# Performance work log

Measured on AMD Instinct MI355X. Metric: run time of the kernel, lower is better.

Reference implementation:

```python
import jax, jax.numpy as jnp
import numpy as np

K, STRIDE, PAD, DIL = 3, 1, 1, 1


def setup_inputs() -> dict:
    key = jax.random.key(0)
    k0, k1, k2, k3, k4 = jax.random.split(key, 5)
    B, Cin, Cout, H, W = 16, 64, 64, 64, 64
    x = jax.random.normal(k0, (B, Cin, H, W), dtype=jnp.float32)
    # NOTE: the torch module zero-inits conv_offset; we use small random
    # weights so the deformable sampling path is actually exercised.
    w_off = jax.random.normal(k1, (2 * K * K, Cin, K, K), dtype=jnp.float32) * 0.01
    b_off = jax.random.normal(k2, (2 * K * K,), dtype=jnp.float32) * 0.01
    fan_in = Cin * K * K
    w_dcn = jax.random.normal(k3, (Cout, Cin, K, K), dtype=jnp.float32) / np.sqrt(fan_in)
    b_dcn = jax.random.normal(k4, (Cout,), dtype=jnp.float32) * 0.01
    return {"x": x, "w_off": w_off, "b_off": b_off, "w_dcn": w_dcn, "b_dcn": b_dcn}


def _conv2d(x, w, b, stride, pad):
    out = jax.lax.conv_general_dilated(
        x, w, window_strides=(stride, stride), padding=[(pad, pad), (pad, pad)],
        dimension_numbers=("NCHW", "OIHW", "NCHW"))
    return out + b[None, :, None, None]


def _deform_conv(x, offset, w, b, stride, pad, dil):
    # torchvision-style DeformConv2d, groups=1, no modulation mask.
    B, Cin, H, W = x.shape
    Cout = w.shape[0]
    Ho = (H + 2 * pad - dil * (K - 1) - 1) // stride + 1
    Wo = (W + 2 * pad - dil * (K - 1) - 1) // stride + 1
    KK = K * K
    # base sampling grid: p0 + dilation*kernel_tap + learned offset
    oy = (jnp.arange(Ho) * stride - pad).astype(x.dtype)
    ox = (jnp.arange(Wo) * stride - pad).astype(x.dtype)
    ky, kx = jnp.meshgrid(jnp.arange(K), jnp.arange(K), indexing="ij")
    ky = (ky * dil).reshape(-1).astype(x.dtype)  # [KK], row (y) of tap
    kx = (kx * dil).reshape(-1).astype(x.dtype)
    # offset channel layout: [y_0, x_0, y_1, x_1, ...] -> [B, KK, 2, Ho, Wo]
    off = offset.reshape(B, KK, 2, Ho, Wo)
    py = off[:, :, 0] + ky[None, :, None, None] + oy[None, None, :, None]  # [B,KK,Ho,Wo]
    px = off[:, :, 1] + kx[None, :, None, None] + ox[None, None, None, :]
    y0 = jnp.floor(py)
    x0 = jnp.floor(px)
    wy1 = py - y0
    wx1 = px - x0
    wy0 = 1.0 - wy1
    wx0 = 1.0 - wx1
    x_flat = x.reshape(B, Cin, H * W)

    def gather(yi, xi):
        valid = (yi >= 0) & (yi < H) & (xi >= 0) & (xi < W)  # zero padding outside
        yc = jnp.clip(yi, 0, H - 1).astype(jnp.int32)
        xc = jnp.clip(xi, 0, W - 1).astype(jnp.int32)
        idx = (yc * W + xc).reshape(B, 1, -1)
        v = jnp.take_along_axis(x_flat, idx, axis=2).reshape(B, Cin, KK, Ho, Wo)
        return v * valid.astype(x.dtype).reshape(B, 1, KK, Ho, Wo)

    cols = (gather(y0, x0) * (wy0 * wx0)[:, None]
            + gather(y0, x0 + 1) * (wy0 * wx1)[:, None]
            + gather(y0 + 1, x0) * (wy1 * wx0)[:, None]
            + gather(y0 + 1, x0 + 1) * (wy1 * wx1)[:, None])  # [B,Cin,KK,Ho,Wo]
    out = jnp.einsum("bckhw,ock->bohw", cols, w.reshape(Cout, Cin, KK))
    return out + b[None, :, None, None]


def reference(x, w_off, b_off, w_dcn, b_dcn):
    offset = _conv2d(x, w_off, b_off, STRIDE, PAD)
    return _deform_conv(x, offset, w_dcn, b_dcn, STRIDE, PAD, DIL)
```

## Files before the change

kernel.cpp:

```cpp
#include <hip/hip_runtime.h>
#include <hip/hip_fp16.h>


#define KOFF 18
#define CTS  136
#define GSTR 33

#define W2T_HALFS    (18 * 64 * 32)
#define WOFF2T_HALFS (18 * 32 * 32)
#define W2T_BYTES    (W2T_HALFS * 2)
#define WOFF2T_OFF   W2T_BYTES
#define X_OFF        (W2T_BYTES + WOFF2T_HALFS * 2)
#define XH_BYTES     (16 * 64 * 64 * 64 * 2)
#define WS_NEED      (X_OFF + XH_BYTES)

typedef _Float16 half8 __attribute__((ext_vector_type(8)));
typedef float floatx4 __attribute__((ext_vector_type(4)));

union H8 { half8 v; __half2 h2[4]; uint4 u; };

__global__ void prep(const float* __restrict__ x,
                     const float* __restrict__ w_dcn,
                     const float* __restrict__ w_off,
                     _Float16* __restrict__ w2t,
                     _Float16* __restrict__ woff2t,
                     _Float16* __restrict__ xh) {
    const int bi = blockIdx.x;
    const int t  = threadIdx.x;
    if (bi < 1024) {
        const int b = bi >> 6, y = bi & 63;
        __shared__ __align__(16) _Float16 tile[64 * 72];
        const int xx = t & 63;
        const int c4 = t >> 6;
        const float* xp = x + (((size_t)b * 64) * 64 + y) * 64;
#pragma unroll
        for (int p = 0; p < 16; ++p) {
            int cin = p * 4 + c4;
            tile[xx * 72 + cin] = (_Float16)xp[(size_t)cin * 4096 + xx];
        }
        __syncthreads();
        const int oct = t & 7;
        const int xl  = t >> 3;
        _Float16* op = xh + ((((size_t)b * 64 + y) * 64) << 6);
#pragma unroll
        for (int p = 0; p < 2; ++p) {
            int xr = p * 32 + xl;
            half8 v = *(const half8*)&tile[xr * 72 + oct * 8];
            *(half8*)&op[(size_t)xr * 64 + oct * 8] = v;
        }
    } else {
        int e = (bi - 1024) * 256 + t;
        if (e < W2T_HALFS) {
            int kl = e & 31, co = (e >> 5) & 63, i = e >> 11;
            int tap = i >> 1, cin = (i & 1) * 32 + kl;
            w2t[e] = (_Float16)w_dcn[co * 576 + cin * 9 + tap];
        } else {
            int e2 = e - W2T_HALFS;
            int kl = e2 & 31, co = (e2 >> 5) & 31, i = e2 >> 10;
            int tap = i >> 1, cin = (i & 1) * 32 + kl;
            woff2t[e2] = (co < KOFF) ? (_Float16)w_off[co * 576 + cin * 9 + tap]
                                     : (_Float16)0.f;
        }
    }
}

__launch_bounds__(256, 4)
__global__ void dcn_main(const _Float16* __restrict__ xh,
                         const _Float16* __restrict__ w2t,
                         const _Float16* __restrict__ woff2t,
                         const float* __restrict__ b_off,
                         const float* __restrict__ b_dcn,
                         float* __restrict__ out) {
    const int bid = blockIdx.x;
    const int s   = bid >> 3;
    const int b   = ((bid & 7) << 1) | (s >> 7);
    const int ho  = (s >> 1) & 63;
    const int hlf = s & 1;
    const int t    = threadIdx.x;
    const int lane = t & 63;
    const int wid  = __builtin_amdgcn_readfirstlane(t >> 6);
    const int r    = lane & 15;
    const int q    = lane >> 4;
    const int gpx  = t >> 3;
    const int oct  = t & 7;
    const int pxg  = hlf * 32;

    __shared__ __align__(16) _Float16 colsT[2][32 * CTS];
    __shared__ __align__(16) float    offlds[KOFF * 32];
    __shared__ __align__(16) uint4    grecL[9 * GSTR];

    const _Float16* xb = xh + ((size_t)b << 18);
    const char* xpb = (const char*)xb;

    {
        floatx4 am = {0.f, 0.f, 0.f, 0.f};
        const int m = wid & 1, n = wid >> 1;

        auto loadS = [&](int tap) -> half8 {
            const int dy = tap / 3, dxk = tap - dy * 3;
            const int y  = ho + dy - 1;
            const int xc = pxg + gpx + dxk - 1;
            half8 v = {};
            if (((unsigned)y < 64u) && ((unsigned)xc < 64u))
                v = *(const half8*)&xb[(((size_t)y * 64 + xc) << 6) + oct * 8];
            return v;
        };
        auto loadWA = [&](int i) -> half8 {
            return *(const half8*)&woff2t[i * 1024 + (m * 16 + r) * 32 + q * 8];
        };

        {
            half8 s0 = loadS(0), s1 = loadS(1);
            *(half8*)&colsT[0][gpx * CTS + oct * 8]      = s0;
            *(half8*)&colsT[0][gpx * CTS + 64 + oct * 8] = s1;
        }
        __syncthreads();
#pragma unroll
        for (int p = 0; p < 5; ++p) {
            half8 sn0, sn1;
            if (p < 4) {
                sn0 = loadS(2 * p + 2);
                if (p < 3) sn1 = loadS(2 * p + 3);
            }
            const int nkg = (p < 4) ? 4 : 2;
#pragma unroll
            for (int kg = 0; kg < 4; ++kg) {
                if (kg < nkg) {
                    half8 a  = loadWA(4 * p + kg);
                    half8 bf = *(const half8*)&colsT[p & 1][(n * 16 + r) * CTS
                                                            + kg * 32 + q * 8];
                    am = __builtin_amdgcn_mfma_f32_16x16x32_f16(a, bf, am, 0, 0, 0);
                }
            }
            if (p < 4) {
                *(half8*)&colsT[(p + 1) & 1][gpx * CTS + oct * 8] = sn0;
                if (p < 3)
                    *(half8*)&colsT[(p + 1) & 1][gpx * CTS + 64 + oct * 8] = sn1;
                __syncthreads();
            }
        }
#pragma unroll
        for (int reg = 0; reg < 4; ++reg) {
            int co = m * 16 + q * 4 + reg;
            if (co < KOFF)
                offlds[co * 32 + n * 16 + r] = am[reg] + b_off[co];
        }
    }
    __syncthreads();

    for (int e = t; e < 9 * 32; e += 256) {
        int tap = e >> 5, px = e & 31;
        float offy = offlds[(2 * tap) * 32 + px];
        float offx = offlds[(2 * tap + 1) * 32 + px];
        float py  = offy + (float)(tap / 3) + (float)(ho - 1);
        float pxf = offx + (float)(tap % 3) + (float)(pxg + px - 1);
        float fy = floorf(py), fx = floorf(pxf);
        int y0 = (int)fy, x0 = (int)fx;
        float wy1 = py - fy, wx1 = pxf - fx;
        float wy0 = 1.f - wy1, wx0 = 1.f - wx1;
        bool y0ok = ((unsigned)y0 < 64u);
        bool x0ok = ((unsigned)x0 < 64u);
        bool y1ok = ((unsigned)(y0 + 1) < 64u);
        bool x1ok = ((unsigned)(x0 + 1) < 64u);
        float w00 = (y0ok && x0ok) ? wy0 * wx0 : 0.f;
        float w01 = (y0ok && x1ok) ? wy0 * wx1 : 0.f;
        float w10 = (y1ok && x0ok) ? wy1 * wx0 : 0.f;
        float w11 = (y1ok && x1ok) ? wy1 * wx1 : 0.f;
        int yc0 = min(max(y0, 0), 63);
        int xc0 = min(max(x0, 0), 63);
        int yc1 = min(max(y0 + 1, 0), 63);
        int xc1 = min(max(x0 + 1, 0), 63);
        union { __half2 h; unsigned u; } c0, c1;
        c0.h = __floats2half2_rn(w00, w01);
        c1.h = __floats2half2_rn(w10, w11);
        uint4 rec;
        rec.x = (unsigned)(yc0 * 64 + xc0)
              | ((unsigned)(xc1 - xc0) << 12)
              | ((unsigned)(yc1 - yc0) << 13);
        rec.y = c0.u;
        rec.z = c1.u;
        rec.w = 0u;
        grecL[tap * GSTR + px] = rec;
    }
    __syncthreads();

    floatx4 acc0 = {0.f, 0.f, 0.f, 0.f};
    floatx4 acc1 = {0.f, 0.f, 0.f, 0.f};

    struct GP { H8 v[8]; unsigned wy0, wz0, wy1, wz1; };

    auto loadPairB = [&](int p) -> GP {
        GP g;
#pragma unroll
        for (int l = 0; l < 2; ++l) {
            int tap = 2 * p + l;
            if (tap < 9) {
                uint4 rec = grecL[tap * GSTR + gpx];
                unsigned a00 = (rec.x & 0xfffu) * 128u + (unsigned)oct * 16u;
                unsigned dx128  = ((rec.x >> 12) & 1u) * 128u;
                unsigned dy8192 = ((rec.x >> 13) & 1u) * 8192u;
                g.v[4 * l + 0].v = *(const half8*)(xpb + a00);
                g.v[4 * l + 1].v = *(const half8*)(xpb + a00 + dx128);
                g.v[4 * l + 2].v = *(const half8*)(xpb + a00 + dy8192);
                g.v[4 * l + 3].v = *(const half8*)(xpb + a00 + dy8192 + dx128);
                if (l == 0) { g.wy0 = rec.y; g.wz0 = rec.z; }
                else        { g.wy1 = rec.y; g.wz1 = rec.z; }
            }
        }
        return g;
    };
    auto storePairB = [&](int p, int buf, GP& g) {
#pragma unroll
        for (int l = 0; l < 2; ++l) {
            int tap = 2 * p + l;
            if (tap < 9) {
                union { unsigned u; __half2 h; } cy, cz;
                cy.u = l ? g.wy1 : g.wy0;
                cz.u = l ? g.wz1 : g.wz0;
                __half2 W00 = __half2half2(__low2half(cy.h));
                __half2 W01 = __half2half2(__high2half(cy.h));
                __half2 W10 = __half2half2(__low2half(cz.h));
                __half2 W11 = __half2half2(__high2half(cz.h));
                H8 res;
#pragma unroll
                for (int c = 0; c < 4; ++c) {
                    __half2 aa = __hmul2(g.v[4 * l + 0].h2[c], W00);
                    aa = __hfma2(g.v[4 * l + 1].h2[c], W01, aa);
                    aa = __hfma2(g.v[4 * l + 2].h2[c], W10, aa);
                    aa = __hfma2(g.v[4 * l + 3].h2[c], W11, aa);
                    res.h2[c] = aa;
                }
                *(half8*)&colsT[buf][gpx * CTS + l * 64 + oct * 8] = res.v;
            }
        }
    };
    auto loadW = [&](int i) -> half8 {
        return *(const half8*)&w2t[(size_t)i * 2048 + (wid * 16 + r) * 32 + q * 8];
    };

    {
        GP g0 = loadPairB(0);
        storePairB(0, 0, g0);
    }
    half8 wf[4];
#pragma unroll
    for (int kg = 0; kg < 4; ++kg) wf[kg] = loadW(kg);
    __syncthreads();

#pragma unroll
    for (int p = 0; p < 5; ++p) {
        GP gn;
        half8 wfn[4];
        if (p < 4) {
            gn = loadPairB(p + 1);
#pragma unroll
            for (int kg = 0; kg < 4; ++kg)
                if (4 * (p + 1) + kg < 18) wfn[kg] = loadW(4 * (p + 1) + kg);
        }
        const int nkg = (p < 4) ? 4 : 2;
#pragma unroll
        for (int kg = 0; kg < 4; ++kg) {
            if (kg < nkg) {
                half8 b0 = *(const half8*)&colsT[p & 1][r * CTS + kg * 32 + q * 8];
                half8 b1 = *(const half8*)&colsT[p & 1][(16 + r) * CTS + kg * 32 + q * 8];
                acc0 = __builtin_amdgcn_mfma_f32_16x16x32_f16(wf[kg], b0, acc0, 0, 0, 0);
                acc1 = __builtin_amdgcn_mfma_f32_16x16x32_f16(wf[kg], b1, acc1, 0, 0, 0);
            }
        }
        if (p < 4) {
            storePairB(p + 1, (p + 1) & 1, gn);
#pragma unroll
            for (int kg = 0; kg < 4; ++kg) wf[kg] = wfn[kg];
            __syncthreads();
        }
    }

#pragma unroll
    for (int reg = 0; reg < 4; ++reg) {
        int co = wid * 16 + q * 4 + reg;
        float bias = b_dcn[co];
        size_t o = (((size_t)b * 64 + co) * 64 + ho) * 64 + pxg;
        out[o + r]      = acc0[reg] + bias;
        out[o + 16 + r] = acc1[reg] + bias;
    }
}

#define FCPAD 40
__launch_bounds__(256, 4)
__global__ void dcn_fb(const float* __restrict__ x,
                       const float* __restrict__ w_dcn,
                       const float* __restrict__ w_off,
                       const float* __restrict__ b_off,
                       const float* __restrict__ b_dcn,
                       float* __restrict__ out) {
    const int bid = blockIdx.x;
    const int s   = bid >> 3;
    const int b   = ((bid & 7) << 1) | (s >> 7);
    const int ho  = (s >> 1) & 63;
    const int hlf = s & 1;
    const int t    = threadIdx.x;
    const int lane = t & 63;
    const int wid  = __builtin_amdgcn_readfirstlane(t >> 6);
    const int r    = lane & 15;
    const int q    = lane >> 4;
    const int px   = t & 31;
    const int kq   = t >> 5;

    __shared__ __align__(16) _Float16 colsT[2][32 * FCPAD];
    __shared__ __align__(16) float    offlds[KOFF * 32];

    const float* xb = x + (size_t)b * 64 * 4096;
    const int pxg = hlf * 32;

    {
        floatx4 am = {0.f, 0.f, 0.f, 0.f};
        const int m = wid & 1, n = wid >> 1;
        auto stageA = [&](int i) {
            const int tap = i >> 1;
            const int dy = tap / 3, dxk = tap - dy * 3;
            const int y  = ho + dy - 1;
            const int xc = pxg + px + dxk - 1;
            const bool ok = ((unsigned)y < 64u) && ((unsigned)xc < 64u);
            const float* xp = xb + ((size_t)((i & 1) * 32 + kq * 4)) * 4096
                                 + y * 64 + xc;
            float va[4];
#pragma unroll
            for (int j = 0; j < 4; ++j) va[j] = ok ? xp[(size_t)j * 4096] : 0.f;
#pragma unroll
            for (int j = 0; j < 4; ++j)
                colsT[i & 1][px * FCPAD + kq * 4 + j] = (_Float16)va[j];
        };
        auto loadA = [&](int i) -> half8 {
            const int tap = i >> 1;
            const int cin0 = (i & 1) * 32 + q * 8;
            const int co = m * 16 + r;
            half8 v;
#pragma unroll
            for (int j = 0; j < 8; ++j)
                v[j] = (co < KOFF) ? (_Float16)w_off[co * 576 + (cin0 + j) * 9 + tap]
                                   : (_Float16)0.f;
            return v;
        };
        stageA(0);
        __syncthreads();
#pragma unroll
        for (int i = 0; i < 18; ++i) {
            if (i < 17) stageA(i + 1);
            half8 a = loadA(i);
            half8 bfr = *(const half8*)&colsT[i & 1][(n * 16 + r) * FCPAD + q * 8];
            am = __builtin_amdgcn_mfma_f32_16x16x32_f16(a, bfr, am, 0, 0, 0);
            __syncthreads();
        }
#pragma unroll
        for (int reg = 0; reg < 4; ++reg) {
            int co = m * 16 + q * 4 + reg;
            if (co < KOFF)
                offlds[co * 32 + (n * 16 + r)] = am[reg] + b_off[co];
        }
    }
    __syncthreads();

    unsigned rmeta[9], rw0[9], rw1[9];
#pragma unroll
    for (int tap = 0; tap < 9; ++tap) {
        float offy = offlds[(2 * tap) * 32 + px];
        float offx = offlds[(2 * tap + 1) * 32 + px];
        float py  = offy + (float)(tap / 3) + (float)(ho - 1);
        float pxf = offx + (float)(tap % 3) + (float)(pxg + px - 1);
        float fy = floorf(py), fx = floorf(pxf);
        int y0 = (int)fy, x0 = (int)fx;
        float wy1 = py - fy, wx1 = pxf - fx;
        float wy0 = 1.f - wy1, wx0 = 1.f - wx1;
        bool y0ok = ((unsigned)y0 < 64u);
        bool x0ok = ((unsigned)x0 < 64u);
        bool y1ok = ((unsigned)(y0 + 1) < 64u);
        bool x1ok = ((unsigned)(x0 + 1) < 64u);
        float w00 = (y0ok && x0ok) ? wy0 * wx0 : 0.f;
        float w01 = (y0ok && x1ok) ? wy0 * wx1 : 0.f;
        float w10 = (y1ok && x0ok) ? wy1 * wx0 : 0.f;
        float w11 = (y1ok && x1ok) ? wy1 * wx1 : 0.f;
        int yc0 = min(max(y0, 0), 63);
        int xc0 = min(max(x0, 0), 63);
        int yc1 = min(max(y0 + 1, 0), 63);
        int xc1 = min(max(x0 + 1, 0), 63);
        union { __half2 h; unsigned u; } c0, c1;
        c0.h = __floats2half2_rn(w00, w01);
        c1.h = __floats2half2_rn(w10, w11);
        rmeta[tap] = (unsigned)(yc0 * 64 + xc0)
                   | ((unsigned)(xc1 - xc0) << 12)
                   | ((unsigned)(yc1 - yc0) << 13);
        rw0[tap] = c0.u;
        rw1[tap] = c1.u;
    }

    floatx4 acc0 = {0.f, 0.f, 0.f, 0.f};
    floatx4 acc1 = {0.f, 0.f, 0.f, 0.f};

    auto gather = [&](int i) {
        const int tap = i >> 1;
        const unsigned m = rmeta[tap];
        const unsigned a00 = (m & 0xfffu) << 2;
        const unsigned a01 = a00 + ((m >> 10) & 4u);
        const unsigned a10 = a00 + ((m >> 5) & 256u);
        const unsigned a11 = a10 + ((m >> 10) & 4u);
        const char* base = (const char*)xb
                         + ((size_t)((i & 1) * 32 + kq * 4)) * 16384;
        float v00[4], v01[4], v10[4], v11[4];
#pragma unroll
        for (int j = 0; j < 4; ++j) {
            const char* xp = base + (size_t)j * 16384;
            v00[j] = *(const float*)(xp + a00);
            v01[j] = *(const float*)(xp + a01);
            v10[j] = *(const float*)(xp + a10);
            v11[j] = *(const float*)(xp + a11);
        }
        union { unsigned u; __half2 h; } c0, c1;
        c0.u = rw0[tap]; c1.u = rw1[tap];
        const float wA = __half2float(c0.h.x), wB = __half2float(c0.h.y);
        const float wC = __half2float(c1.h.x), wD = __half2float(c1.h.y);
#pragma unroll
        for (int j = 0; j < 4; ++j)
            colsT[i & 1][px * FCPAD + kq * 4 + j] =
                (_Float16)(v00[j] * wA + v01[j] * wB + v10[j] * wC + v11[j] * wD);
    };

    auto load_af = [&](int i) -> half8 {
        const int tap = i >> 1;
        const int cin0 = (i & 1) * 32 + q * 8;
        half8 v;
#pragma unroll
        for (int j = 0; j < 8; ++j)
            v[j] = (_Float16)w_dcn[(wid * 16 + r) * 576 + (cin0 + j) * 9 + tap];
        return v;
    };

    gather(0);
    __syncthreads();
#pragma unroll
    for (int i = 0; i < 18; ++i) {
        if (i < 17) gather(i + 1);
        half8 af = load_af(i);
        half8 b0 = *(const half8*)&colsT[i & 1][r * FCPAD + q * 8];
        half8 b1 = *(const half8*)&colsT[i & 1][(16 + r) * FCPAD + q * 8];
        acc0 = __builtin_amdgcn_mfma_f32_16x16x32_f16(af, b0, acc0, 0, 0, 0);
        acc1 = __builtin_amdgcn_mfma_f32_16x16x32_f16(af, b1, acc1, 0, 0, 0);
        if (i < 17) __syncthreads();
    }

#pragma unroll
    for (int reg = 0; reg < 4; ++reg) {
        int co = wid * 16 + q * 4 + reg;
        float bias = b_dcn[co];
        size_t o = (((size_t)b * 64 + co) * 64 + ho) * 64 + pxg;
        out[o + r]      = acc0[reg] + bias;
        out[o + 16 + r] = acc1[reg] + bias;
    }
}

extern "C" void kernel_launch(void* const* d_in, const int* in_sizes, int n_in,
                              void* d_out, int out_size, void* d_ws, size_t ws_size,
                              hipStream_t stream) {
    const float* x     = (const float*)d_in[0];
    const float* w_off = (const float*)d_in[1];
    const float* b_off = (const float*)d_in[2];
    const float* w_dcn = (const float*)d_in[3];
    const float* b_dcn = (const float*)d_in[4];
    float* out = (float*)d_out;

    char* ws = (char*)d_ws;
    _Float16* w2t    = (_Float16*)ws;
    _Float16* woff2t = (_Float16*)(ws + WOFF2T_OFF);
    _Float16* xh     = (_Float16*)(ws + X_OFF);

    if (ws_size >= (size_t)WS_NEED) {
        prep<<<1240, 256, 0, stream>>>(x, w_dcn, w_off, w2t, woff2t, xh);
        dcn_main<<<2048, 256, 0, stream>>>(xh, w2t, woff2t, b_off, b_dcn, out);
    } else {
        dcn_fb<<<2048, 256, 0, stream>>>(x, w_dcn, w_off, b_off, b_dcn, out);
    }
}
```

Measured before the change: 107.6 us.

## Prefetch gathers two stages ahead and use LDS-only barriers

New measurement: 108.5 us. About the same (+0.8%).

```diff
diff --git a/kernel.cpp b/kernel.cpp
--- a/kernel.cpp
+++ b/kernel.cpp
@@ -18,6 +18,11 @@
 typedef float floatx4 __attribute__((ext_vector_type(4)));
 
 union H8 { half8 v; __half2 h2[4]; uint4 u; };
+
+#define LBAR() do { \
+    asm volatile("s_waitcnt lgkmcnt(0)" ::: "memory"); \
+    __builtin_amdgcn_s_barrier(); \
+} while (0)
 
 __global__ void prep(const float* __restrict__ x,
                      const float* __restrict__ w_dcn,
@@ -109,19 +114,17 @@
             return *(const half8*)&woff2t[i * 1024 + (m * 16 + r) * 32 + q * 8];
         };
 
+        half8 t0, t1;
         {
             half8 s0 = loadS(0), s1 = loadS(1);
+            t0 = loadS(2);
+            t1 = loadS(3);
             *(half8*)&colsT[0][gpx * CTS + oct * 8]      = s0;
             *(half8*)&colsT[0][gpx * CTS + 64 + oct * 8] = s1;
         }
-        __syncthreads();
+        LBAR();
 #pragma unroll
         for (int p = 0; p < 5; ++p) {
-            half8 sn0, sn1;
-            if (p < 4) {
-                sn0 = loadS(2 * p + 2);
-                if (p < 3) sn1 = loadS(2 * p + 3);
-            }
             const int nkg = (p < 4) ? 4 : 2;
 #pragma unroll
             for (int kg = 0; kg < 4; ++kg) {
@@ -133,10 +136,14 @@
                 }
             }
             if (p < 4) {
-                *(half8*)&colsT[(p + 1) & 1][gpx * CTS + oct * 8] = sn0;
+                *(half8*)&colsT[(p + 1) & 1][gpx * CTS + oct * 8] = t0;
                 if (p < 3)
-                    *(half8*)&colsT[(p + 1) & 1][gpx * CTS + 64 + oct * 8] = sn1;
-                __syncthreads();
+                    *(half8*)&colsT[(p + 1) & 1][gpx * CTS + 64 + oct * 8] = t1;
+                if (p < 3) {
+                    t0 = loadS(2 * p + 4);
+                    if (p < 2) t1 = loadS(2 * p + 5);
+                }
+                LBAR();
             }
         }
 #pragma unroll
@@ -146,7 +153,7 @@
                 offlds[co * 32 + n * 16 + r] = am[reg] + b_off[co];
         }
     }
-    __syncthreads();
+    LBAR();
 
     for (int e = t; e < 9 * 32; e += 256) {
         int tap = e >> 5, px = e & 31;
@@ -182,7 +189,7 @@
         rec.w = 0u;
         grecL[tap * GSTR + px] = rec;
     }
-    __syncthreads();
+    LBAR();
 
     floatx4 acc0 = {0.f, 0.f, 0.f, 0.f};
     floatx4 acc1 = {0.f, 0.f, 0.f, 0.f};
@@ -242,17 +249,16 @@
         GP g0 = loadPairB(0);
         storePairB(0, 0, g0);
     }
+    GP gcur = loadPairB(1);
     half8 wf[4];
 #pragma unroll
     for (int kg = 0; kg < 4; ++kg) wf[kg] = loadW(kg);
-    __syncthreads();
+    LBAR();
 
 #pragma unroll
     for (int p = 0; p < 5; ++p) {
-        GP gn;
         half8 wfn[4];
         if (p < 4) {
-            gn = loadPairB(p + 1);
 #pragma unroll
             for (int kg = 0; kg < 4; ++kg)
                 if (4 * (p + 1) + kg < 18) wfn[kg] = loadW(4 * (p + 1) + kg);
@@ -268,10 +274,11 @@
             }
         }
         if (p < 4) {
-            storePairB(p + 1, (p + 1) & 1, gn);
+            storePairB(p + 1, (p + 1) & 1, gcur);
+            if (p < 3) gcur = loadPairB(p + 2);
 #pragma unroll
             for (int kg = 0; kg < 4; ++kg) wf[kg] = wfn[kg];
-            __syncthreads();
+            LBAR();
         }
     }
 
```

## Split offset conv into separate kernel and stage full im2col tile in LDS

Applied to the files above, without the earlier changes.

After: 110.8 us. +3.0%, slower.

```diff
diff --git a/kernel.cpp b/kernel.cpp
--- a/kernel.cpp
+++ b/kernel.cpp
@@ -4,7 +4,7 @@
 
 #define KOFF 18
 #define CTS  136
-#define GSTR 33
+#define CS9  584
 
 #define W2T_HALFS    (18 * 64 * 32)
 #define WOFF2T_HALFS (18 * 32 * 32)
@@ -12,7 +12,11 @@
 #define WOFF2T_OFF   W2T_BYTES
 #define X_OFF        (W2T_BYTES + WOFF2T_HALFS * 2)
 #define XH_BYTES     (16 * 64 * 64 * 64 * 2)
-#define WS_NEED      (X_OFF + XH_BYTES)
+#define GM_OFF       (X_OFF + XH_BYTES)
+#define GM_BYTES     (2048 * 288 * 4)
+#define GW_OFF       (GM_OFF + GM_BYTES)
+#define GW_BYTES     (2048 * 288 * 8)
+#define WS_NEED      (GW_OFF + GW_BYTES)
 
 typedef _Float16 half8 __attribute__((ext_vector_type(8)));
 typedef float floatx4 __attribute__((ext_vector_type(4)));
@@ -65,12 +69,11 @@
 }
 
 __launch_bounds__(256, 4)
-__global__ void dcn_main(const _Float16* __restrict__ xh,
-                         const _Float16* __restrict__ w2t,
-                         const _Float16* __restrict__ woff2t,
-                         const float* __restrict__ b_off,
-                         const float* __restrict__ b_dcn,
-                         float* __restrict__ out) {
+__global__ void offs_k(const _Float16* __restrict__ xh,
+                       const _Float16* __restrict__ woff2t,
+                       const float* __restrict__ b_off,
+                       unsigned int* __restrict__ gm,
+                       uint2* __restrict__ gw) {
     const int bid = blockIdx.x;
     const int s   = bid >> 3;
     const int b   = ((bid & 7) << 1) | (s >> 7);
@@ -87,10 +90,8 @@
 
     __shared__ __align__(16) _Float16 colsT[2][32 * CTS];
     __shared__ __align__(16) float    offlds[KOFF * 32];
-    __shared__ __align__(16) uint4    grecL[9 * GSTR];
 
     const _Float16* xb = xh + ((size_t)b << 18);
-    const char* xpb = (const char*)xb;
 
     {
         floatx4 am = {0.f, 0.f, 0.f, 0.f};
@@ -173,43 +174,78 @@
         union { __half2 h; unsigned u; } c0, c1;
         c0.h = __floats2half2_rn(w00, w01);
         c1.h = __floats2half2_rn(w10, w11);
-        uint4 rec;
-        rec.x = (unsigned)(yc0 * 64 + xc0)
-              | ((unsigned)(xc1 - xc0) << 12)
-              | ((unsigned)(yc1 - yc0) << 13);
-        rec.y = c0.u;
-        rec.z = c1.u;
-        rec.w = 0u;
-        grecL[tap * GSTR + px] = rec;
+        unsigned meta = (unsigned)(yc0 * 64 + xc0)
+                      | ((unsigned)(xc1 - xc0) << 12)
+                      | ((unsigned)(yc1 - yc0) << 13);
+        gm[(size_t)bid * 288 + e] = meta;
+        gw[(size_t)bid * 288 + e] = make_uint2(c0.u, c1.u);
+    }
+}
+
+__launch_bounds__(256, 4)
+__global__ void dcn_main(const _Float16* __restrict__ xh,
+                         const _Float16* __restrict__ w2t,
+                         const unsigned int* __restrict__ gm,
+                         const uint2* __restrict__ gw,
+                         const float* __restrict__ b_dcn,
+                         float* __restrict__ out) {
+    const int bid = blockIdx.x;
+    const int s   = bid >> 3;
+    const int b   = ((bid & 7) << 1) | (s >> 7);
+    const int ho  = (s >> 1) & 63;
+    const int hlf = s & 1;
+    const int t    = threadIdx.x;
+    const int lane = t & 63;
+    const int wid  = __builtin_amdgcn_readfirstlane(t >> 6);
+    const int r    = lane & 15;
+    const int q    = lane >> 4;
+    const int gpx  = t >> 3;
+    const int oct  = t & 7;
+    const int pxg  = hlf * 32;
+
+    __shared__ __align__(16) _Float16 cols[32 * CS9];
+    __shared__ __align__(16) uint2        gwL[288];
+    __shared__ __align__(16) unsigned int gmL[288];
+
+    const _Float16* xb = xh + ((size_t)b << 18);
+    const char* xpb = (const char*)xb;
+
+    {
+        const unsigned int* gmp = gm + (size_t)bid * 288;
+        const uint2*        gwp = gw + (size_t)bid * 288;
+        gmL[t] = gmp[t];
+        gwL[t] = gwp[t];
+        if (t < 32) {
+            gmL[256 + t] = gmp[256 + t];
+            gwL[256 + t] = gwp[256 + t];
+        }
     }
     __syncthreads();
 
-    floatx4 acc0 = {0.f, 0.f, 0.f, 0.f};
-    floatx4 acc1 = {0.f, 0.f, 0.f, 0.f};
-
     struct GP { H8 v[8]; unsigned wy0, wz0, wy1, wz1; };
 
-    auto loadPairB = [&](int p) -> GP {
+    auto loadPair = [&](int p) -> GP {
         GP g;
 #pragma unroll
         for (int l = 0; l < 2; ++l) {
             int tap = 2 * p + l;
             if (tap < 9) {
-                uint4 rec = grecL[tap * GSTR + gpx];
-                unsigned a00 = (rec.x & 0xfffu) * 128u + (unsigned)oct * 16u;
-                unsigned dx128  = ((rec.x >> 12) & 1u) * 128u;
-                unsigned dy8192 = ((rec.x >> 13) & 1u) * 8192u;
+                unsigned meta = gmL[tap * 32 + gpx];
+                uint2    w    = gwL[tap * 32 + gpx];
+                unsigned a00 = (meta & 0xfffu) * 128u + (unsigned)oct * 16u;
+                unsigned dx128  = ((meta >> 12) & 1u) * 128u;
+                unsigned dy8192 = ((meta >> 13) & 1u) * 8192u;
                 g.v[4 * l + 0].v = *(const half8*)(xpb + a00);
                 g.v[4 * l + 1].v = *(const half8*)(xpb + a00 + dx128);
                 g.v[4 * l + 2].v = *(const half8*)(xpb + a00 + dy8192);
                 g.v[4 * l + 3].v = *(const half8*)(xpb + a00 + dy8192 + dx128);
-                if (l == 0) { g.wy0 = rec.y; g.wz0 = rec.z; }
-                else        { g.wy1 = rec.y; g.wz1 = rec.z; }
+                if (l == 0) { g.wy0 = w.x; g.wz0 = w.y; }
+                else        { g.wy1 = w.x; g.wz1 = w.y; }
             }
         }
         return g;
     };
-    auto storePairB = [&](int p, int buf, GP& g) {
+    auto storePair = [&](int p, GP& g) {
 #pragma unroll
         for (int l = 0; l < 2; ++l) {
             int tap = 2 * p + l;
@@ -230,49 +266,39 @@
                     aa = __hfma2(g.v[4 * l + 3].h2[c], W11, aa);
                     res.h2[c] = aa;
                 }
-                *(half8*)&colsT[buf][gpx * CTS + l * 64 + oct * 8] = res.v;
+                *(half8*)&cols[gpx * CS9 + tap * 64 + oct * 8] = res.v;
             }
         }
     };
+
+    {
+        GP gcur = loadPair(0);
+#pragma unroll
+        for (int p = 0; p < 5; ++p) {
+            GP gn;
+            if (p < 4) gn = loadPair(p + 1);
+            storePair(p, gcur);
+            if (p < 4) gcur = gn;
+        }
+    }
+    __syncthreads();
+
     auto loadW = [&](int i) -> half8 {
         return *(const half8*)&w2t[(size_t)i * 2048 + (wid * 16 + r) * 32 + q * 8];
     };
 
-    {
-        GP g0 = loadPairB(0);
-        storePairB(0, 0, g0);
-    }
-    half8 wf[4];
-#pragma unroll
-    for (int kg = 0; kg < 4; ++kg) wf[kg] = loadW(kg);
-    __syncthreads();
-
-#pragma unroll
-    for (int p = 0; p < 5; ++p) {
-        GP gn;
-        half8 wfn[4];
-        if (p < 4) {
-            gn = loadPairB(p + 1);
-#pragma unroll
-            for (int kg = 0; kg < 4; ++kg)
-                if (4 * (p + 1) + kg < 18) wfn[kg] = loadW(4 * (p + 1) + kg);
-        }
-        const int nkg = (p < 4) ? 4 : 2;
-#pragma unroll
-        for (int kg = 0; kg < 4; ++kg) {
-            if (kg < nkg) {
-                half8 b0 = *(const half8*)&colsT[p & 1][r * CTS + kg * 32 + q * 8];
-                half8 b1 = *(const half8*)&colsT[p & 1][(16 + r) * CTS + kg * 32 + q * 8];
-                acc0 = __builtin_amdgcn_mfma_f32_16x16x32_f16(wf[kg], b0, acc0, 0, 0, 0);
-                acc1 = __builtin_amdgcn_mfma_f32_16x16x32_f16(wf[kg], b1, acc1, 0, 0, 0);
-            }
-        }
-        if (p < 4) {
-            storePairB(p + 1, (p + 1) & 1, gn);
-#pragma unroll
-            for (int kg = 0; kg < 4; ++kg) wf[kg] = wfn[kg];
-            __syncthreads();
-        }
+    floatx4 acc0 = {0.f, 0.f, 0.f, 0.f};
+    floatx4 acc1 = {0.f, 0.f, 0.f, 0.f};
+    half8 wfc = loadW(0);
+#pragma unroll
+    for (int i = 0; i < 18; ++i) {
+        half8 wfn;
+        if (i < 17) wfn = loadW(i + 1);
+        half8 b0 = *(const half8*)&cols[r * CS9 + i * 32 + q * 8];
+        half8 b1 = *(const half8*)&cols[(16 + r) * CS9 + i * 32 + q * 8];
+        acc0 = __builtin_amdgcn_mfma_f32_16x16x32_f16(wfc, b0, acc0, 0, 0, 0);
+        acc1 = __builtin_amdgcn_mfma_f32_16x16x32_f16(wfc, b1, acc1, 0, 0, 0);
+        if (i < 17) wfc = wfn;
     }
 
 #pragma unroll
@@ -471,10 +497,13 @@
     _Float16* w2t    = (_Float16*)ws;
     _Float16* woff2t = (_Float16*)(ws + WOFF2T_OFF);
     _Float16* xh     = (_Float16*)(ws + X_OFF);
+    unsigned int* gm = (unsigned int*)(ws + GM_OFF);
+    uint2*        gw = (uint2*)(ws + GW_OFF);
 
     if (ws_size >= (size_t)WS_NEED) {
         prep<<<1240, 256, 0, stream>>>(x, w_dcn, w_off, w2t, woff2t, xh);
-        dcn_main<<<2048, 256, 0, stream>>>(xh, w2t, woff2t, b_off, b_dcn, out);
+        offs_k<<<2048, 256, 0, stream>>>(xh, woff2t, b_off, gm, gw);
+        dcn_main<<<2048, 256, 0, stream>>>(xh, w2t, gm, gw, b_dcn, out);
     } else {
         dcn_fb<<<2048, 256, 0, stream>>>(x, w_dcn, w_off, b_off, b_dcn, out);
     }
```

## Stage swizzled input halo in LDS and serve conv and bilinear gathers from it

Applied to the files above, without the earlier changes.

Measured after the change: 104.5 us. 2.9% less time.

```diff
diff --git a/kernel.cpp b/kernel.cpp
--- a/kernel.cpp
+++ b/kernel.cpp
@@ -3,8 +3,10 @@
 
 
 #define KOFF 18
-#define CTS  136
-#define GSTR 33
+#define HROWS 5
+#define HCOLS 37
+#define HALO_HALFS (HROWS * HCOLS * 64)
+#define CS3 192
 
 #define W2T_HALFS    (18 * 64 * 32)
 #define WOFF2T_HALFS (18 * 32 * 32)
@@ -65,12 +67,12 @@
 }
 
 __launch_bounds__(256, 4)
-__global__ void dcn_main(const _Float16* __restrict__ xh,
-                         const _Float16* __restrict__ w2t,
-                         const _Float16* __restrict__ woff2t,
-                         const float* __restrict__ b_off,
-                         const float* __restrict__ b_dcn,
-                         float* __restrict__ out) {
+__global__ void dcn_one(const _Float16* __restrict__ xh,
+                        const _Float16* __restrict__ w2t,
+                        const _Float16* __restrict__ woff2t,
+                        const float* __restrict__ b_off,
+                        const float* __restrict__ b_dcn,
+                        float* __restrict__ out) {
     const int bid = blockIdx.x;
     const int s   = bid >> 3;
     const int b   = ((bid & 7) << 1) | (s >> 7);
@@ -85,59 +87,44 @@
     const int oct  = t & 7;
     const int pxg  = hlf * 32;
 
-    __shared__ __align__(16) _Float16 colsT[2][32 * CTS];
-    __shared__ __align__(16) float    offlds[KOFF * 32];
-    __shared__ __align__(16) uint4    grecL[9 * GSTR];
+    __shared__ __align__(16) _Float16 haloL[HALO_HALFS];
+    __shared__ __align__(16) _Float16 colsL[32 * CS3];
+    __shared__ __align__(16) unsigned int gmetaL[288];
+    __shared__ __align__(16) uint2        gwL[288];
+    float* offlds = (float*)colsL;
 
     const _Float16* xb = xh + ((size_t)b << 18);
     const char* xpb = (const char*)xb;
+
+    for (int e = t; e < HROWS * HCOLS * 8; e += 256) {
+        int sl   = e & 7;
+        int rest = e >> 3;
+        int hx = rest % HCOLS;
+        int hy = rest / HCOLS;
+        int y = ho - 2 + hy;
+        int xx = pxg - 2 + hx;
+        half8 v = {};
+        if (((unsigned)y < 64u) && ((unsigned)xx < 64u)) {
+            int oc = sl ^ (hx & 7);
+            v = *(const half8*)&xb[(((size_t)(y * 64 + xx)) << 6) + oc * 8];
+        }
+        *(half8*)&haloL[(size_t)(rest * 8 + sl) * 8] = v;
+    }
+    __syncthreads();
 
     {
         floatx4 am = {0.f, 0.f, 0.f, 0.f};
         const int m = wid & 1, n = wid >> 1;
-
-        auto loadS = [&](int tap) -> half8 {
-            const int dy = tap / 3, dxk = tap - dy * 3;
-            const int y  = ho + dy - 1;
-            const int xc = pxg + gpx + dxk - 1;
-            half8 v = {};
-            if (((unsigned)y < 64u) && ((unsigned)xc < 64u))
-                v = *(const half8*)&xb[(((size_t)y * 64 + xc) << 6) + oct * 8];
-            return v;
-        };
-        auto loadWA = [&](int i) -> half8 {
-            return *(const half8*)&woff2t[i * 1024 + (m * 16 + r) * 32 + q * 8];
-        };
-
-        {
-            half8 s0 = loadS(0), s1 = loadS(1);
-            *(half8*)&colsT[0][gpx * CTS + oct * 8]      = s0;
-            *(half8*)&colsT[0][gpx * CTS + 64 + oct * 8] = s1;
-        }
-        __syncthreads();
-#pragma unroll
-        for (int p = 0; p < 5; ++p) {
-            half8 sn0, sn1;
-            if (p < 4) {
-                sn0 = loadS(2 * p + 2);
-                if (p < 3) sn1 = loadS(2 * p + 3);
-            }
-            const int nkg = (p < 4) ? 4 : 2;
-#pragma unroll
-            for (int kg = 0; kg < 4; ++kg) {
-                if (kg < nkg) {
-                    half8 a  = loadWA(4 * p + kg);
-                    half8 bf = *(const half8*)&colsT[p & 1][(n * 16 + r) * CTS
-                                                            + kg * 32 + q * 8];
-                    am = __builtin_amdgcn_mfma_f32_16x16x32_f16(a, bf, am, 0, 0, 0);
-                }
-            }
-            if (p < 4) {
-                *(half8*)&colsT[(p + 1) & 1][gpx * CTS + oct * 8] = sn0;
-                if (p < 3)
-                    *(half8*)&colsT[(p + 1) & 1][gpx * CTS + 64 + oct * 8] = sn1;
-                __syncthreads();
-            }
+#pragma unroll
+        for (int i = 0; i < 18; ++i) {
+            const int tap = i >> 1, ch = i & 1;
+            const int hy = tap / 3 + 1;
+            const int px = n * 16 + r;
+            const int hx = px + (tap % 3) + 1;
+            const int sl = (ch * 4 + q) ^ (hx & 7);
+            half8 bf = *(const half8*)&haloL[((hy * HCOLS + hx) * 8 + sl) * 8];
+            half8 a  = *(const half8*)&woff2t[i * 1024 + (m * 16 + r) * 32 + q * 8];
+            am = __builtin_amdgcn_mfma_f32_16x16x32_f16(a, bf, am, 0, 0, 0);
         }
 #pragma unroll
         for (int reg = 0; reg < 4; ++reg) {
@@ -173,106 +160,91 @@
         union { __half2 h; unsigned u; } c0, c1;
         c0.h = __floats2half2_rn(w00, w01);
         c1.h = __floats2half2_rn(w10, w11);
-        uint4 rec;
-        rec.x = (unsigned)(yc0 * 64 + xc0)
-              | ((unsigned)(xc1 - xc0) << 12)
-              | ((unsigned)(yc1 - yc0) << 13);
-        rec.y = c0.u;
-        rec.z = c1.u;
-        rec.w = 0u;
-        grecL[tap * GSTR + px] = rec;
+        bool fast = (yc0 >= ho - 2) && (yc1 <= ho + 2)
+                 && (xc0 >= pxg - 2) && (xc1 <= pxg + 34);
+        unsigned meta;
+        if (fast) {
+            unsigned hy0 = (unsigned)(yc0 - (ho - 2));
+            unsigned hx0 = (unsigned)(xc0 - (pxg - 2));
+            meta = 0x80000000u | hx0 | (hy0 << 8)
+                 | ((unsigned)(xc1 - xc0) << 16)
+                 | ((unsigned)(yc1 - yc0) << 17);
+        } else {
+            meta = (unsigned)(yc0 * 64 + xc0)
+                 | ((unsigned)(xc1 - xc0) << 12)
+                 | ((unsigned)(yc1 - yc0) << 13);
+        }
+        gmetaL[e] = meta;
+        gwL[e]    = make_uint2(c0.u, c1.u);
     }
     __syncthreads();
 
     floatx4 acc0 = {0.f, 0.f, 0.f, 0.f};
     floatx4 acc1 = {0.f, 0.f, 0.f, 0.f};
 
-    struct GP { H8 v[8]; unsigned wy0, wz0, wy1, wz1; };
-
-    auto loadPairB = [&](int p) -> GP {
-        GP g;
-#pragma unroll
-        for (int l = 0; l < 2; ++l) {
-            int tap = 2 * p + l;
-            if (tap < 9) {
-                uint4 rec = grecL[tap * GSTR + gpx];
-                unsigned a00 = (rec.x & 0xfffu) * 128u + (unsigned)oct * 16u;
-                unsigned dx128  = ((rec.x >> 12) & 1u) * 128u;
-                unsigned dy8192 = ((rec.x >> 13) & 1u) * 8192u;
-                g.v[4 * l + 0].v = *(const half8*)(xpb + a00);
-                g.v[4 * l + 1].v = *(const half8*)(xpb + a00 + dx128);
-                g.v[4 * l + 2].v = *(const half8*)(xpb + a00 + dy8192);
-                g.v[4 * l + 3].v = *(const half8*)(xpb + a00 + dy8192 + dx128);
-                if (l == 0) { g.wy0 = rec.y; g.wz0 = rec.z; }
-                else        { g.wy1 = rec.y; g.wz1 = rec.z; }
+#pragma unroll
+    for (int c = 0; c < 3; ++c) {
+#pragma unroll
+        for (int u3 = 0; u3 < 3; ++u3) {
+            const int tap = c * 3 + u3;
+            unsigned meta = gmetaL[tap * 32 + gpx];
+            uint2    wr   = gwL[tap * 32 + gpx];
+            H8 v00, v01, v10, v11;
+            if (meta & 0x80000000u) {
+                int hx0 = (int)(meta & 63u);
+                int hy0 = (int)((meta >> 8) & 7u);
+                int dx  = (int)((meta >> 16) & 1u);
+                int dy  = (int)((meta >> 17) & 1u);
+                int b0i = hy0 * HCOLS + hx0;
+                int s0  = oct ^ (hx0 & 7);
+                int s1  = oct ^ ((hx0 + dx) & 7);
+                v00.v = *(const half8*)&haloL[(b0i * 8 + s0) * 8];
+                v01.v = *(const half8*)&haloL[((b0i + dx) * 8 + s1) * 8];
+                v10.v = *(const half8*)&haloL[((b0i + dy * HCOLS) * 8 + s0) * 8];
+                v11.v = *(const half8*)&haloL[((b0i + dy * HCOLS + dx) * 8 + s1) * 8];
+            } else {
+                unsigned a00 = (meta & 0xfffu) * 128u + (unsigned)oct * 16u;
+                unsigned dx128  = ((meta >> 12) & 1u) * 128u;
+                unsigned dy8192 = ((meta >> 13) & 1u) * 8192u;
+                v00.v = *(const half8*)(xpb + a00);
+                v01.v = *(const half8*)(xpb + a00 + dx128);
+                v10.v = *(const half8*)(xpb + a00 + dy8192);
+                v11.v = *(const half8*)(xpb + a00 + dy8192 + dx128);
             }
-        }
-        return g;
-    };
-    auto storePairB = [&](int p, int buf, GP& g) {
-#pragma unroll
-        for (int l = 0; l < 2; ++l) {
-            int tap = 2 * p + l;
-            if (tap < 9) {
-                union { unsigned u; __half2 h; } cy, cz;
-                cy.u = l ? g.wy1 : g.wy0;
-                cz.u = l ? g.wz1 : g.wz0;
-                __half2 W00 = __half2half2(__low2half(cy.h));
-                __half2 W01 = __half2half2(__high2half(cy.h));
-                __half2 W10 = __half2half2(__low2half(cz.h));
-                __half2 W11 = __half2half2(__high2half(cz.h));
-                H8 res;
-#pragma unroll
-                for (int c = 0; c < 4; ++c) {
-                    __half2 aa = __hmul2(g.v[4 * l + 0].h2[c], W00);
-                    aa = __hfma2(g.v[4 * l + 1].h2[c], W01, aa);
-                    aa = __hfma2(g.v[4 * l + 2].h2[c], W10, aa);
-                    aa = __hfma2(g.v[4 * l + 3].h2[c], W11, aa);
-                    res.h2[c] = aa;
-                }
-                *(half8*)&colsT[buf][gpx * CTS + l * 64 + oct * 8] = res.v;
+            union { unsigned u; __half2 h; } cy, cz;
+            cy.u = wr.x;
+            cz.u = wr.y;
+            __half2 W00 = __half2half2(__low2half(cy.h));
+            __half2 W01 = __half2half2(__high2half(cy.h));
+            __half2 W10 = __half2half2(__low2half(cz.h));
+            __half2 W11 = __half2half2(__high2half(cz.h));
+            H8 res;
+#pragma unroll
+            for (int cc = 0; cc < 4; ++cc) {
+                __half2 aa = __hmul2(v00.h2[cc], W00);
+                aa = __hfma2(v01.h2[cc], W01, aa);
+                aa = __hfma2(v10.h2[cc], W10, aa);
+                aa = __hfma2(v11.h2[cc], W11, aa);
+                res.h2[cc] = aa;
             }
-        }
-    };
-    auto loadW = [&](int i) -> half8 {
-        return *(const half8*)&w2t[(size_t)i * 2048 + (wid * 16 + r) * 32 + q * 8];
-    };
-
-    {
-        GP g0 = loadPairB(0);
-        storePairB(0, 0, g0);
-    }
-    half8 wf[4];
-#pragma unroll
-    for (int kg = 0; kg < 4; ++kg) wf[kg] = loadW(kg);
-    __syncthreads();
-
-#pragma unroll
-    for (int p = 0; p < 5; ++p) {
-        GP gn;
-        half8 wfn[4];
-        if (p < 4) {
-            gn = loadPairB(p + 1);
-#pragma unroll
-            for (int kg = 0; kg < 4; ++kg)
-                if (4 * (p + 1) + kg < 18) wfn[kg] = loadW(4 * (p + 1) + kg);
-        }
-        const int nkg = (p < 4) ? 4 : 2;
-#pragma unroll
-        for (int kg = 0; kg < 4; ++kg) {
-            if (kg < nkg) {
-                half8 b0 = *(const half8*)&colsT[p & 1][r * CTS + kg * 32 + q * 8];
-                half8 b1 = *(const half8*)&colsT[p & 1][(16 + r) * CTS + kg * 32 + q * 8];
-                acc0 = __builtin_amdgcn_mfma_f32_16x16x32_f16(wf[kg], b0, acc0, 0, 0, 0);
-                acc1 = __builtin_amdgcn_mfma_f32_16x16x32_f16(wf[kg], b1, acc1, 0, 0, 0);
-            }
-        }
-        if (p < 4) {
-            storePairB(p + 1, (p + 1) & 1, gn);
-#pragma unroll
-            for (int kg = 0; kg < 4; ++kg) wf[kg] = wfn[kg];
-            __syncthreads();
-        }
+            *(half8*)&colsL[gpx * CS3 + u3 * 64 + (oct ^ (gpx & 7)) * 8] = res.v;
+        }
+        half8 wf6[6];
+#pragma unroll
+        for (int u = 0; u < 6; ++u)
+            wf6[u] = *(const half8*)&w2t[(size_t)(c * 6 + u) * 2048
+                                         + (wid * 16 + r) * 32 + q * 8];
+        __syncthreads();
+#pragma unroll
+        for (int u = 0; u < 6; ++u) {
+            const int u3 = u >> 1, ch = u & 1;
+            const int sl = (ch * 4 + q) ^ (r & 7);
+            half8 b0 = *(const half8*)&colsL[r * CS3 + u3 * 64 + sl * 8];
+            half8 b1 = *(const half8*)&colsL[(16 + r) * CS3 + u3 * 64 + sl * 8];
+            acc0 = __builtin_amdgcn_mfma_f32_16x16x32_f16(wf6[u], b0, acc0, 0, 0, 0);
+            acc1 = __builtin_amdgcn_mfma_f32_16x16x32_f16(wf6[u], b1, acc1, 0, 0, 0);
+        }
+        if (c < 2) __syncthreads();
     }
 
 #pragma unroll
@@ -474,7 +446,7 @@
 
     if (ws_size >= (size_t)WS_NEED) {
         prep<<<1240, 256, 0, stream>>>(x, w_dcn, w_off, w2t, woff2t, xh);
-        dcn_main<<<2048, 256, 0, stream>>>(xh, w2t, woff2t, b_off, b_dcn, out);
+        dcn_one<<<2048, 256, 0, stream>>>(xh, w2t, woff2t, b_off, b_dcn, out);
     } else {
         dcn_fb<<<2048, 256, 0, stream>>>(x, w_dcn, w_off, b_off, b_dcn, out);
     }
```
